# Optimization experiments

Hardware: AMD Instinct MI355X
Metric: run time of the kernel (lower is better)

Reference implementation:

```python
import jax, jax.numpy as jnp
import numpy as np

B, NEG = 2, 16            # queries, negatives per query
N, E, D = 10000, 80000, 128  # nodes, edges, feature dim (in_dim == out_dim)
NUM_REL = 237
L = 3                     # PNA layers
NODE_RATIO = 0.1
K = max(1, int(NODE_RATIO * N))  # static top-k: every repeated graph has exactly N nodes
EPS = 1e-5


def _score(hidden, rel, lin_W, lin_b, m1_W, m1_b, m2_W, m2_b):
    heur = jnp.concatenate([hidden, rel], axis=-1) @ lin_W + lin_b
    x = heur * hidden
    h = jax.nn.relu(x @ m1_W + m1_b)
    return jnp.squeeze(h @ m2_W + m2_b, -1)


def _pna_conv(hidden, src, dst, emask, deg, pre_W, pre_b, post_W, post_b, out_W, out_b):
    """PNA layer with mean/max/min/std aggregators and identity/amplification/attenuation
    scalers, restricted to edges where emask is True. deg is the (clamped >=1) degree used
    by the scalers."""
    BN = hidden.shape[0]
    # message: pre-linear on [x_i (target), x_j (source)] per edge  -> (Erep, D)
    m = jnp.concatenate([hidden[dst], hidden[src]], axis=-1) @ pre_W + pre_b
    w = emask.astype(hidden.dtype)[:, None]
    cnt = jax.ops.segment_sum(emask.astype(hidden.dtype), dst, num_segments=BN)
    denom = jnp.maximum(cnt, 1.0)[:, None]
    s1 = jax.ops.segment_sum(m * w, dst, num_segments=BN)
    s2 = jax.ops.segment_sum(m * m * w, dst, num_segments=BN)
    mean = s1 / denom
    var = jax.nn.relu(s2 / denom - mean * mean)
    std = jnp.sqrt(var + EPS)
    has = (cnt > 0)[:, None]
    mx = jnp.where(has, jax.ops.segment_max(jnp.where(emask[:, None], m, -jnp.inf), dst, num_segments=BN), 0.0)
    mn = jnp.where(has, jax.ops.segment_min(jnp.where(emask[:, None], m, jnp.inf), dst, num_segments=BN), 0.0)
    agg = jnp.concatenate([mean, mx, mn, std], axis=-1)           # (BN, 4D)
    logd = jnp.log(deg + 1.0)                                     # deg >= 1 -> logd > 0
    avg_log = jnp.mean(logd)
    agg = jnp.concatenate([agg, agg * (logd / avg_log)[:, None], agg * (avg_log / logd)[:, None]], axis=-1)  # (BN, 12D)
    return (agg @ post_W + post_b) @ out_W + out_b


def _forward(h_index, r_index, t_index, hidden_states, edge_index, rel_embedding,
             lin_W, lin_b, m1_W, m1_b, m2_W, m2_b, pre_W, pre_b, post_W, post_b, out_W, out_b):
    sc = (lin_W, lin_b, m1_W, m1_b, m2_W, m2_b)
    # negative_sample_to_tail
    is_t_neg = jnp.all(h_index == h_index[:, :1], axis=-1, keepdims=True)
    h_idx = jnp.where(is_t_neg, h_index, t_index)
    t_idx = jnp.where(is_t_neg, t_index, h_index)
    r_idx = jnp.where(is_t_neg, r_index, r_index + NUM_REL)
    # repeat_graph
    offsets = jnp.arange(B, dtype=h_idx.dtype) * N               # (B,)
    src = jnp.tile(edge_index[0], B) + jnp.repeat(offsets, E)    # (B*E,)
    dst = jnp.tile(edge_index[1], B) + jnp.repeat(offsets, E)
    BN = B * N
    rel_embeds = rel_embedding[r_idx[:, 0]].astype(hidden_states.dtype)  # (B, D)
    flat_h = h_idx[:, 0] + offsets
    flat_t = t_idx[:, 0] + offsets
    # literal `repeat_interleave(N, dim=0)[:B]` quirk -> row arange(B)//N of gathered embs
    sel = jnp.arange(B) // N
    h_vals = hidden_states[h_idx[:, 0]][sel]                     # (B, D)
    t_vals = hidden_states[t_idx[:, 0]][sel]
    # init_input_embeds: boundary condition + initial score at head nodes
    boundary = jnp.zeros((BN, D), hidden_states.dtype).at[flat_t].set(t_vals).at[flat_h].set(h_vals)
    score = jnp.zeros(BN, jnp.float32).at[flat_h].set(_score(h_vals, rel_embeds, *sc))
    hidden = boundary
    rel_per_node = jnp.repeat(rel_embeds, N, axis=0)             # (BN, D), rel_embeds[batch_rep]
    rows = jnp.arange(B)[:, None]
    for l in range(L):
        # select_edges_pyg with degree_ratio=1.0: all out-edges of per-graph top-k nodes
        _, idx = jax.lax.top_k(score.reshape(B, N), K)           # (B, K)
        node_sel = jnp.zeros((B, N), bool).at[rows, idx].set(True).reshape(-1)
        emask = node_sel[src]                                    # (B*E,) selected-edge mask
        out_deg = jax.ops.segment_sum(emask.astype(jnp.float32), src, num_segments=BN)
        deg_sub = jnp.maximum(out_deg.astype(hidden.dtype), 1.0)
        new_hidden = _pna_conv(hidden, src, dst, emask, deg_sub,
                               pre_W[l], pre_b[l], post_W[l], post_b[l], out_W[l], out_b[l])
        # residual only for nodes with selected outgoing edges
        hidden = jnp.where((out_deg > 0)[:, None], hidden + new_hidden, hidden)
        score = _score(hidden, rel_per_node, *sc)
    # read out scores at (repeated) tail indices -> (B, NEG)
    return score[t_idx + offsets[:, None]]


def setup_inputs() -> dict:
    key = jax.random.key(0)
    ks = jax.random.split(key, 14)
    s = 0.05
    hi = jax.random.randint(ks[0], (B, 1), 0, N)
    h_index = jnp.tile(hi, (1, NEG))                 # constant per row (assert in forward)
    r0 = jax.random.randint(ks[1], (B, 1), 0, NUM_REL)
    r_index = jnp.tile(r0, (1, NEG))                 # constant per row (assert in forward)
    t_index = jax.random.randint(ks[2], (B, NEG), 0, N)
    hidden_states = jax.random.normal(ks[3], (N, D), jnp.float32)
    edge_index = jax.random.randint(ks[4], (2, E), 0, N)
    return {
        "h_index": h_index, "r_index": r_index, "t_index": t_index,
        "hidden_states": hidden_states, "edge_index": edge_index,
        "rel_embedding": jax.random.normal(ks[5], (2 * NUM_REL, D), jnp.float32) * s,
        "lin_W": jax.random.normal(ks[6], (2 * D, D), jnp.float32) * s, "lin_b": jnp.zeros(D, jnp.float32),
        "m1_W": jax.random.normal(ks[7], (D, D), jnp.float32) * s, "m1_b": jnp.zeros(D, jnp.float32),
        "m2_W": jax.random.normal(ks[8], (D, 1), jnp.float32) * s, "m2_b": jnp.zeros(1, jnp.float32),
        "pre_W": jax.random.normal(ks[9], (L, 2 * D, D), jnp.float32) * s, "pre_b": jnp.zeros((L, D), jnp.float32),
        "post_W": jax.random.normal(ks[10], (L, 12 * D, D), jnp.float32) * s, "post_b": jnp.zeros((L, D), jnp.float32),
        "out_W": jax.random.normal(ks[11], (L, D, D), jnp.float32) * s, "out_b": jnp.zeros((L, D), jnp.float32),
    }


def reference(h_index, r_index, t_index, hidden_states, edge_index, rel_embedding,
              lin_W, lin_b, m1_W, m1_b, m2_W, m2_b, pre_W, pre_b, post_W, post_b, out_W, out_b):
    return _forward(h_index, r_index, t_index, hidden_states, edge_index, rel_embedding,
                    lin_W, lin_b, m1_W, m1_b, m2_W, m2_b, pre_W, pre_b, post_W, post_b, out_W, out_b)
```

## Files before the change

### kernel.cpp

```cpp
#include <hip/hip_runtime.h>
#include <math.h>

#define Bq 2
#define NEG 16
#define Nn 10000
#define Ee 80000
#define Dd 128
#define NUM_REL 237
#define Ll 3
#define K_SEL 1000
#define BN (Bq*Nn)
#define EPSV 1e-5f
#define MAXACT 2048
#define MAXTOUCH 8192
#define SELCAP 3328
#define LN2F 0.69314718056f

constexpr size_t HID_OFF   = 0;
constexpr size_t SCORE_OFF = HID_OFF   + (size_t)BN*Dd*4;
constexpr size_t CVEC_OFF  = SCORE_OFF + (size_t)BN*4;
constexpr size_t HDR_OFF   = CVEC_OFF  + (size_t)Bq*Dd*4;
constexpr size_t THR_OFF   = HDR_OFF   + 64*4;
constexpr size_t SEL_OFF   = THR_OFF   + Bq*8;
constexpr size_t DEG_OFF   = SEL_OFF   + (size_t)BN*4;
constexpr size_t SLOT_OFF  = DEG_OFF   + (size_t)BN*4;
constexpr size_t CNT_OFF   = SLOT_OFF  + (size_t)BN*4;
constexpr size_t SDEG_OFF  = CNT_OFF   + (size_t)MAXACT*4;
constexpr size_t S1_OFF    = SDEG_OFF  + (size_t)MAXACT*4;
constexpr size_t S2_OFF    = S1_OFF    + (size_t)MAXACT*Dd*4;
constexpr size_t MXB_OFF   = S2_OFF    + (size_t)MAXACT*Dd*4;
constexpr size_t MNB_OFF   = MXB_OFF   + (size_t)MAXACT*Dd*4;
constexpr size_t TPART_OFF = MNB_OFF   + (size_t)MAXACT*Dd*4;
constexpr size_t ALIST_OFF = TPART_OFF + (size_t)4*MAXACT*Dd*4;
constexpr size_t FLAG_OFF  = ALIST_OFF + (size_t)MAXACT*4;
constexpr size_t TLIST_OFF = FLAG_OFF  + (size_t)BN*4;
constexpr size_t EDGE_OFF  = TLIST_OFF + (size_t)MAXTOUCH*4;
constexpr size_t CTR_OFF   = EDGE_OFF  + (size_t)Bq*Ee*2*4;

__device__ __forceinline__ unsigned encf(float f){
  unsigned u = __float_as_uint(f);
  return (u & 0x80000000u) ? ~u : (u | 0x80000000u);
}
__device__ __forceinline__ float decf(unsigned e){
  unsigned u = (e & 0x80000000u) ? (e & 0x7FFFFFFFu) : ~e;
  return __uint_as_float(u);
}
__device__ __forceinline__ unsigned long long make_key(float f, int i){
  unsigned d = ~encf(f);
  return ((unsigned long long)d << 32) | (unsigned)i;
}

__global__ void k_zero(float* hidden, unsigned* flag){
  int i = blockIdx.x*blockDim.x + threadIdx.x;
  if (i < BN*Dd/4) ((float4*)hidden)[i] = make_float4(0.f,0.f,0.f,0.f);
  if (i < BN) flag[i] = 0u;
}

__global__ __launch_bounds__(256) void k_prep(
    const int* h_index, const int* r_index, const int* t_index,
    const float* hidden_states, const float* rel_embedding,
    const float* lin_W, const float* lin_b, const float* m1_W, const float* m1_b,
    const float* m2_W, const float* m2_b,
    int* hdr, float* cvec, float* hidden, float* score,
    unsigned* flag, int* tlist, unsigned* ctr){
  __shared__ int sh_fh[Bq], sh_ft[Bq], sh_r0[Bq], sh_hsrc, sh_tsrc;
  __shared__ float s_relv[Bq][Dd], s_cvec[Bq][Dd], s_hv[Dd], s_x[Bq][Dd], s_p[Bq][Dd];
  __shared__ float s_s0[Dd];
  __shared__ float sc0_sh;
  int tid = threadIdx.x;
  if (tid == 0){
    int n = 0;
    for (int b=0;b<Bq;b++){
      bool eq = true;
      for (int j=1;j<NEG;j++) eq = eq && (h_index[b*NEG+j]==h_index[b*NEG]);
      int h0 = eq ? h_index[b*NEG] : t_index[b*NEG];
      int t0 = eq ? t_index[b*NEG] : h_index[b*NEG];
      int r0 = eq ? r_index[b*NEG] : r_index[b*NEG] + NUM_REL;
      sh_fh[b] = h0 + b*Nn; sh_ft[b] = t0 + b*Nn; sh_r0[b] = r0;
      hdr[0+b] = sh_fh[b]; hdr[2+b] = sh_ft[b];
      for (int j=0;j<NEG;j++){
        int tj = eq ? t_index[b*NEG+j] : h_index[b*NEG+j];
        hdr[4 + b*NEG + j] = tj + b*Nn;
      }
      if (b==0){ sh_hsrc = h0; sh_tsrc = t0; }
      if (!flag[sh_ft[b]]){ flag[sh_ft[b]] = 1u; tlist[n++] = sh_ft[b]; }
      if (!flag[sh_fh[b]]){ flag[sh_fh[b]] = 1u; tlist[n++] = sh_fh[b]; }
    }
    ctr[3] = (unsigned)n;
  }
  __syncthreads();
  int b = tid >> 7, d = tid & 127;
  s_relv[b][d] = rel_embedding[(size_t)sh_r0[b]*Dd + d];
  if (b == 0){
    s_hv[d] = hidden_states[(size_t)sh_hsrc*Dd + d];
    s_s0[d] = fmaxf(m1_b[d], 0.f) * m2_W[d];
  }
  __syncthreads();
  if (tid == 0){
    float s = m2_b[0];
    for (int k=0;k<Dd;k++) s += s_s0[k];
    sc0_sh = s;
    ctr[4] = __float_as_uint(s);
  }
  float acc = lin_b[d];
  #pragma unroll 8
  for (int k=0;k<Dd;k++) acc += s_relv[b][k]*lin_W[(Dd+k)*Dd + d];
  s_cvec[b][d] = acc; cvec[b*Dd+d] = acc;
  hidden[(size_t)sh_ft[b]*Dd + d] = hidden_states[(size_t)sh_tsrc*Dd + d];
  hidden[(size_t)sh_fh[b]*Dd + d] = hidden_states[(size_t)sh_hsrc*Dd + d];
  __syncthreads();
  float sc0 = sc0_sh;
  for (int i = tid; i < BN; i += 256) score[i] = sc0;
  float hv = s_hv[d];
  float heur = s_cvec[b][d];
  #pragma unroll 8
  for (int k=0;k<Dd;k++) heur += s_hv[k]*lin_W[k*Dd + d];
  s_x[b][d] = heur * hv;
  __syncthreads();
  float a2 = m1_b[d];
  #pragma unroll 8
  for (int k=0;k<Dd;k++) a2 += s_x[b][k]*m1_W[k*Dd + d];
  s_p[b][d] = fmaxf(a2, 0.f) * m2_W[d];
  __syncthreads();
  if (tid < Bq){
    float s = m2_b[0];
    for (int k=0;k<Dd;k++) s += s_p[tid][k];
    score[sh_fh[tid]] = s;
  }
}

__global__ __launch_bounds__(256) void k_select(
    const float* score, const int* tlist, const unsigned* ctr,
    unsigned long long* thr){
  int b = blockIdx.x;
  int nt = (int)ctr[3];
  unsigned d0 = ~encf(__uint_as_float(ctr[4]));
  __shared__ unsigned sd[SELCAP];
  __shared__ unsigned short sidx[SELCAP];
  __shared__ unsigned hist[256], histT[256];
  __shared__ int ntb_sh;
  __shared__ unsigned long long pref_sh;
  __shared__ unsigned kk_sh;
  int tid = threadIdx.x;
  if (tid==0){ ntb_sh = 0; pref_sh = 0ull; kk_sh = K_SEL; }
  __syncthreads();
  int vlo = b*Nn, vhi = vlo + Nn;
  for (int i = tid; i < nt; i += 256){
    int v = tlist[i];
    if (v >= vlo && v < vhi){
      int pos = atomicAdd(&ntb_sh, 1);
      if (pos < SELCAP){
        sd[pos] = ~encf(score[v]);
        sidx[pos] = (unsigned short)(v - vlo);
      }
    }
  }
  __syncthreads();
  int ntb = min(ntb_sh, SELCAP);
  unsigned nvirt = (unsigned)(Nn - ntb);
  for (int pass = 7; pass >= 0; --pass){
    hist[tid] = 0u; histT[tid] = 0u;
    __syncthreads();
    unsigned long long pref = pref_sh;
    int sh_hi = 8*(pass+1);
    for (int j = tid; j < ntb; j += 256){
      unsigned long long key = ((unsigned long long)sd[j] << 32) | (unsigned long long)sidx[j];
      bool ok = (pass==7) || ((key >> sh_hi) == (pref >> sh_hi));
      if (ok) atomicAdd(&hist[(unsigned)(key >> (8*pass)) & 255u], 1u);
      if (pass < 4){
        unsigned idx = sidx[j];
        bool oki = (pass == 3) || ((idx >> sh_hi) == (((unsigned)pref) >> sh_hi));
        if (oki) atomicAdd(&histT[(idx >> (8*pass)) & 255u], 1u);
      }
    }
    __syncthreads();
    if (pass >= 4){
      if (tid == 0){
        unsigned long long keyv_hi = ((unsigned long long)d0 << 32);
        bool ok = (pass==7) || ((keyv_hi >> sh_hi) == (pref >> sh_hi));
        if (ok) atomicAdd(&hist[(d0 >> (8*(pass-4))) & 255u], nvirt);
      }
    } else {
      if ((unsigned)(pref >> 32) == d0){
        unsigned long long hf = 0ull;
        if (pass < 3) hf = (unsigned long long)((((unsigned)pref) >> sh_hi)) << sh_hi;
        unsigned long long lo = hf + ((unsigned long long)tid << (8*pass));
        unsigned long long hi = lo + (1ull << (8*pass));
        unsigned long long nn = (unsigned long long)Nn;
        unsigned long long l2 = lo < nn ? lo : nn;
        unsigned long long h2 = hi < nn ? hi : nn;
        if (h2 > l2){
          unsigned c = (unsigned)(h2 - l2) - histT[tid];
          if (c > 0u) atomicAdd(&hist[tid], c);
        }
      }
    }
    __syncthreads();
    if (tid < 256){
      unsigned kk = kk_sh;
      unsigned cum = 0;
      for (int i=0;i<tid;i++) cum += hist[i];
      unsigned h = hist[tid];
      if (h > 0u && cum < kk && kk <= cum + h){
        pref_sh |= ((unsigned long long)tid) << (8*pass);
        kk_sh = kk - cum;
      }
    }
    __syncthreads();
  }
  if (tid==0) thr[b] = pref_sh;
}

__global__ void k_mask(const float* score, const unsigned long long* thr, unsigned* sel,
                       unsigned* out_deg, float* s1, float* s2,
                       unsigned* mxb, unsigned* mnb, unsigned* cnt, unsigned* ctr){
  int i = blockIdx.x*blockDim.x + threadIdx.x;
  if (i < BN){
    int b = i / Nn; int v = i - b*Nn;
    sel[i] = (make_key(score[i], v) <= thr[b]) ? 1u : 0u;
    out_deg[i] = 0u;
  }
  if (i < MAXACT*Dd){ s1[i]=0.f; s2[i]=0.f; mxb[i]=0u; mnb[i]=0xFFFFFFFFu; }
  if (i < MAXACT) cnt[i]=0u;
  if (i < 3) ctr[i]=0u;
}

__global__ void k_degree(const int* ei, const unsigned* sel, unsigned* out_deg){
  int e = blockIdx.x*blockDim.x + threadIdx.x;
  if (e >= Ee) return;
  int s0 = ei[e];
  #pragma unroll
  for (int b=0;b<Bq;b++){
    int v = s0 + b*Nn;
    if (sel[v]) atomicAdd(&out_deg[v], 1u);
  }
}

__global__ void k_active(const unsigned* out_deg, int* node_slot, int* alist,
                         float* slot_deg, unsigned* ctr, unsigned* flag, int* tlist){
  int v = blockIdx.x*blockDim.x + threadIdx.x;
  if (v >= BN) return;
  unsigned dg = out_deg[v];
  if (dg > 0u){
    int slot = (int)atomicAdd(&ctr[0], 1u);
    alist[slot] = v; node_slot[v] = slot; slot_deg[slot] = (float)dg;
    atomicAdd((float*)&ctr[2], logf((float)dg + 1.0f));
    if (atomicExch(&flag[v], 1u) == 0u){
      int p = (int)atomicAdd(&ctr[3], 1u);
      tlist[p] = v;
    }
  }
}

__global__ void k_edges(const int* ei, const unsigned* sel, const unsigned* out_deg,
                        const int* node_slot, int* edges, unsigned* cnt, unsigned* ctr){
  int e = blockIdx.x*blockDim.x + threadIdx.x;
  if (e >= Ee) return;
  int s0 = ei[e], d0 = ei[Ee + e];
  #pragma unroll
  for (int b=0;b<Bq;b++){
    int s = s0 + b*Nn, dv = d0 + b*Nn;
    if (sel[s] && out_deg[dv] > 0u){
      int slot = node_slot[dv];
      int j = (int)atomicAdd(&ctr[1], 1u);
      edges[2*j] = s; edges[2*j+1] = slot;
      atomicAdd(&cnt[slot], 1u);
    }
  }
}

__global__ __launch_bounds__(128) void k_messages(
    const float* hidden, const int* edges, const int* alist,
    const float* preW, const float* preb,
    float* s1, float* s2, unsigned* mxb, unsigned* mnb, const unsigned* ctr){
  int ne = (int)ctr[1];
  int tid = threadIdx.x;
  __shared__ float sd[4][Dd], ss[4][Dd];
  __shared__ int dsl[4];
  float pb = preb[tid];
  for (int j0 = blockIdx.x*4; j0 < ne; j0 += gridDim.x*4){
    int nv = ne - j0; if (nv > 4) nv = 4;
    if (tid < 4){
      int j = j0 + ((tid < nv) ? tid : 0);
      dsl[tid] = edges[2*j+1];
    }
    #pragma unroll
    for (int e=0;e<4;e++){
      int j = j0 + ((e < nv) ? e : 0);
      int s = edges[2*j];
      int dv = alist[edges[2*j+1]];
      sd[e][tid] = hidden[(size_t)dv*Dd + tid];
      ss[e][tid] = hidden[(size_t)s*Dd + tid];
    }
    __syncthreads();
    float a[4] = {pb, pb, pb, pb};
    #pragma unroll 4
    for (int k=0;k<Dd;k++){
      float w0 = preW[k*Dd + tid];
      float w1 = preW[(Dd+k)*Dd + tid];
      #pragma unroll
      for (int e=0;e<4;e++) a[e] += sd[e][k]*w0 + ss[e][k]*w1;
    }
    for (int e=0;e<nv;e++){
      int dslot = dsl[e];
      atomicAdd(&s1[dslot*Dd + tid], a[e]);
      atomicAdd(&s2[dslot*Dd + tid], a[e]*a[e]);
      atomicMax(&mxb[dslot*Dd + tid], encf(a[e]));
      atomicMin(&mnb[dslot*Dd + tid], encf(a[e]));
    }
    __syncthreads();
  }
}

__global__ __launch_bounds__(512) void k_post(
    const unsigned* cnt, const float* s1, const float* s2,
    const unsigned* mxb, const unsigned* mnb, const float* slot_deg,
    const float* postW, float* tpart, const unsigned* ctr){
  int na = (int)ctr[0];
  int bid = blockIdx.x;
  int tile = bid & 63, ch = bid >> 6;
  if (tile*32 >= na) return;
  float logsum = __uint_as_float(ctr[2]);
  float avg = (logsum + (float)(BN - na)*LN2F) / (float)BN;
  __shared__ float lb[32*136];
  __shared__ float wbuf[3*16*128];
  __shared__ float sden[32];
  __shared__ unsigned shas[32];
  int tid = threadIdx.x;
  if (tid < 32){
    unsigned c = cnt[tile*32 + tid];
    sden[tid] = fmaxf((float)c, 1.0f);
    shas[tid] = c;
  }
  __syncthreads();
  for (int idx = tid; idx < 32*Dd; idx += 512){
    int sl = idx >> 7, kk = idx & 127;
    int gi = (tile*32 + sl)*Dd + kk;
    float den = sden[sl];
    float val;
    if (ch == 0)      val = s1[gi]/den;
    else if (ch == 1) val = shas[sl] ? decf(mxb[gi]) : 0.f;
    else if (ch == 2) val = shas[sl] ? decf(mnb[gi]) : 0.f;
    else {
      float mv = s1[gi]/den;
      float var = s2[gi]/den - mv*mv;
      val = sqrtf(fmaxf(var, 0.f) + EPSV);
    }
    lb[sl*136 + kk] = val;
  }
  int cg = tid & 31, rg = tid >> 5;
  int c0 = cg*4;
  float a0[2][4], a1[2][4], a2[2][4];
  #pragma unroll
  for (int i=0;i<2;i++)
    #pragma unroll
    for (int j=0;j<4;j++){ a0[i][j]=0.f; a1[i][j]=0.f; a2[i][j]=0.f; }
  for (int chunk = 0; chunk < 8; ++chunk){
    #pragma unroll
    for (int i = 0; i < 3; ++i){
      int f = tid + i*512;
      int q = f >> 9, r = f & 511;
      int kk = r >> 5, c4 = r & 31;
      int grow = q*512 + ch*128 + chunk*16 + kk;
      ((float4*)wbuf)[f] = *(const float4*)(postW + (size_t)grow*Dd + c4*4);
    }
    __syncthreads();
    #pragma unroll
    for (int k4 = 0; k4 < 4; ++k4){
      float4 av0 = *(const float4*)&lb[(rg*2+0)*136 + chunk*16 + k4*4];
      float4 av1 = *(const float4*)&lb[(rg*2+1)*136 + chunk*16 + k4*4];
      #pragma unroll
      for (int j = 0; j < 4; ++j){
        int kk = k4*4 + j;
        float4 w0 = *(const float4*)&wbuf[kk*128 + c0];
        float4 w1 = *(const float4*)&wbuf[(16+kk)*128 + c0];
        float4 w2 = *(const float4*)&wbuf[(32+kk)*128 + c0];
        float av[2] = { (&av0.x)[j], (&av1.x)[j] };
        #pragma unroll
        for (int i=0;i<2;i++){
          float a = av[i];
          a0[i][0] += a*w0.x; a0[i][1] += a*w0.y; a0[i][2] += a*w0.z; a0[i][3] += a*w0.w;
          a1[i][0] += a*w1.x; a1[i][1] += a*w1.y; a1[i][2] += a*w1.z; a1[i][3] += a*w1.w;
          a2[i][0] += a*w2.x; a2[i][1] += a*w2.y; a2[i][2] += a*w2.z; a2[i][3] += a*w2.w;
        }
      }
    }
    __syncthreads();
  }
  #pragma unroll
  for (int i=0;i<2;i++){
    int slot = tile*32 + rg*2 + i;
    if (slot < na){
      float dg = slot_deg[slot];
      float logd = logf(dg + 1.f);
      float al = logd/avg, be = avg/logd;
      float4 r;
      r.x = a0[i][0] + al*a1[i][0] + be*a2[i][0];
      r.y = a0[i][1] + al*a1[i][1] + be*a2[i][1];
      r.z = a0[i][2] + al*a1[i][2] + be*a2[i][2];
      r.w = a0[i][3] + al*a1[i][3] + be*a2[i][3];
      *(float4*)(tpart + (size_t)ch*MAXACT*Dd + (size_t)slot*Dd + c0) = r;
    }
  }
}

__global__ __launch_bounds__(256) void k_out_resid(
    const float* tpart, const int* alist, const float* outW, const float* outb,
    const float* postb, float* hidden, const unsigned* ctr){
  int na = (int)ctr[0];
  int tile = blockIdx.x;
  if (tile*32 >= na) return;
  __shared__ float tr[32*136];
  __shared__ float wbuf[16*128];
  int tid = threadIdx.x;
  for (int idx = tid; idx < 32*Dd; idx += 256){
    int sl = idx >> 7, kk = idx & 127;
    size_t o = (size_t)(tile*32 + sl)*Dd + kk;
    tr[sl*136 + kk] = tpart[o] + tpart[(size_t)MAXACT*Dd + o]
                    + tpart[(size_t)2*MAXACT*Dd + o] + tpart[(size_t)3*MAXACT*Dd + o]
                    + postb[kk];
  }
  int cg = tid & 31, rg = tid >> 5;
  int c0 = cg*4;
  float4 ob = *(const float4*)(outb + c0);
  float acc[4][4];
  #pragma unroll
  for (int r=0;r<4;r++){ acc[r][0]=ob.x; acc[r][1]=ob.y; acc[r][2]=ob.z; acc[r][3]=ob.w; }
  for (int chunk = 0; chunk < 8; ++chunk){
    #pragma unroll
    for (int i = 0; i < 2; ++i){
      int f = tid + i*256;
      int kk = f >> 5, c4 = f & 31;
      ((float4*)wbuf)[f] = *(const float4*)(outW + (size_t)(chunk*16 + kk)*Dd + c4*4);
    }
    __syncthreads();
    #pragma unroll
    for (int k4 = 0; k4 < 4; ++k4){
      float4 av[4];
      #pragma unroll
      for (int r=0;r<4;r++)
        av[r] = *(const float4*)&tr[(rg*4+r)*136 + chunk*16 + k4*4];
      #pragma unroll
      for (int j = 0; j < 4; ++j){
        float4 w = *(const float4*)&wbuf[(k4*4+j)*128 + c0];
        #pragma unroll
        for (int r=0;r<4;r++){
          float a = (&av[r].x)[j];
          acc[r][0] += a*w.x; acc[r][1] += a*w.y; acc[r][2] += a*w.z; acc[r][3] += a*w.w;
        }
      }
    }
    __syncthreads();
  }
  #pragma unroll
  for (int r=0;r<4;r++){
    int slot = tile*32 + rg*4 + r;
    if (slot < na){
      int v = alist[slot];
      float* hp = hidden + (size_t)v*Dd + c0;
      float4 h4 = *(float4*)hp;
      h4.x += acc[r][0]; h4.y += acc[r][1]; h4.z += acc[r][2]; h4.w += acc[r][3];
      *(float4*)hp = h4;
    }
  }
}

__global__ __launch_bounds__(256) void k_score(
    const float* hidden, const float* cvec, const float* linW,
    const float* m1W, const float* m1b, const float* m2W, const float* m2b,
    const int* tlist, const unsigned* ctr, float* score,
    const int* ovr, int ovr_n){
  int nt = (ovr_n > 0) ? ovr_n : (int)ctr[3];
  const int* list = (ovr_n > 0) ? ovr : tlist;
  int nb = blockIdx.x * 32;
  if (nb >= nt) return;
  __shared__ float sh[32*Dd];
  __shared__ float sx[32*Dd];
  __shared__ float sc[2*Dd];
  __shared__ int   sv[32];
  __shared__ float red[32*33];
  int tid = threadIdx.x;
  if (tid < 32){
    int idx = nb + tid;
    sv[tid] = (idx < nt) ? list[idx] : list[nb];
  }
  sc[tid] = cvec[tid];
  __syncthreads();
  for (int q = tid; q < 32*32; q += 256){
    int row = q >> 5, f4 = q & 31;
    ((float4*)sh)[row*32 + f4] = ((const float4*)(hidden + (size_t)sv[row]*Dd))[f4];
  }
  __syncthreads();
  int cg = tid & 31, rg = tid >> 5;
  int c0 = cg*4;
  float acc[4][4];
  #pragma unroll
  for (int i=0;i<4;i++){ acc[i][0]=0.f; acc[i][1]=0.f; acc[i][2]=0.f; acc[i][3]=0.f; }
  for (int k4=0;k4<32;k4++){
    float4 av[4];
    #pragma unroll
    for (int i=0;i<4;i++) av[i] = ((float4*)sh)[(rg*4+i)*32 + k4];
    #pragma unroll
    for (int j=0;j<4;j++){
      float4 w = *(const float4*)(linW + (size_t)(k4*4+j)*Dd + c0);
      #pragma unroll
      for (int i=0;i<4;i++){
        float a = (&av[i].x)[j];
        acc[i][0] += a*w.x; acc[i][1] += a*w.y; acc[i][2] += a*w.z; acc[i][3] += a*w.w;
      }
    }
  }
  #pragma unroll
  for (int i=0;i<4;i++){
    int row = rg*4 + i;
    int bb = (sv[row] >= Nn) ? 1 : 0;
    float4 cv = *(float4*)&sc[bb*Dd + c0];
    float4 hv = ((float4*)sh)[row*32 + cg];
    float4 x;
    x.x = (acc[i][0] + cv.x)*hv.x;
    x.y = (acc[i][1] + cv.y)*hv.y;
    x.z = (acc[i][2] + cv.z)*hv.z;
    x.w = (acc[i][3] + cv.w)*hv.w;
    ((float4*)sx)[row*32 + cg] = x;
  }
  __syncthreads();
  #pragma unroll
  for (int i=0;i<4;i++){ acc[i][0]=0.f; acc[i][1]=0.f; acc[i][2]=0.f; acc[i][3]=0.f; }
  for (int k4=0;k4<32;k4++){
    float4 av[4];
    #pragma unroll
    for (int i=0;i<4;i++) av[i] = ((float4*)sx)[(rg*4+i)*32 + k4];
    #pragma unroll
    for (int j=0;j<4;j++){
      float4 w = *(const float4*)(m1W + (size_t)(k4*4+j)*Dd + c0);
      #pragma unroll
      for (int i=0;i<4;i++){
        float a = (&av[i].x)[j];
        acc[i][0] += a*w.x; acc[i][1] += a*w.y; acc[i][2] += a*w.z; acc[i][3] += a*w.w;
      }
    }
  }
  float4 mb = *(const float4*)(m1b + c0);
  float4 mw = *(const float4*)(m2W + c0);
  #pragma unroll
  for (int i=0;i<4;i++){
    float p0 = fmaxf(acc[i][0]+mb.x, 0.f)*mw.x;
    float p1 = fmaxf(acc[i][1]+mb.y, 0.f)*mw.y;
    float p2 = fmaxf(acc[i][2]+mb.z, 0.f)*mw.z;
    float p3 = fmaxf(acc[i][3]+mb.w, 0.f)*mw.w;
    red[(rg*4+i)*33 + cg] = p0+p1+p2+p3;
  }
  __syncthreads();
  if (tid < 32){
    float s = m2b[0];
    for (int g=0; g<32; g++) s += red[tid*33 + g];
    if (nb + tid < nt) score[sv[tid]] = s;
  }
}

__global__ void k_gather(const float* score, const int* hdr, float* out){
  int i = threadIdx.x;
  if (i < Bq*NEG) out[i] = score[hdr[4+i]];
}

extern "C" void kernel_launch(void* const* d_in, const int* in_sizes, int n_in,
                              void* d_out, int out_size, void* d_ws, size_t ws_size,
                              hipStream_t stream){
  const int*   h_index       = (const int*)d_in[0];
  const int*   r_index       = (const int*)d_in[1];
  const int*   t_index       = (const int*)d_in[2];
  const float* hidden_states = (const float*)d_in[3];
  const int*   edge_index    = (const int*)d_in[4];
  const float* rel_embedding = (const float*)d_in[5];
  const float* lin_W  = (const float*)d_in[6];
  const float* lin_b  = (const float*)d_in[7];
  const float* m1_W   = (const float*)d_in[8];
  const float* m1_b   = (const float*)d_in[9];
  const float* m2_W   = (const float*)d_in[10];
  const float* m2_b   = (const float*)d_in[11];
  const float* pre_W  = (const float*)d_in[12];
  const float* pre_b  = (const float*)d_in[13];
  const float* post_W = (const float*)d_in[14];
  const float* post_b = (const float*)d_in[15];
  const float* out_W  = (const float*)d_in[16];
  const float* out_b  = (const float*)d_in[17];

  char* ws = (char*)d_ws;
  float*    hidden   = (float*)(ws + HID_OFF);
  float*    score    = (float*)(ws + SCORE_OFF);
  float*    cvec     = (float*)(ws + CVEC_OFF);
  int*      hdr      = (int*)(ws + HDR_OFF);
  unsigned long long* thr = (unsigned long long*)(ws + THR_OFF);
  unsigned* sel      = (unsigned*)(ws + SEL_OFF);
  unsigned* out_deg  = (unsigned*)(ws + DEG_OFF);
  int*      node_slot= (int*)(ws + SLOT_OFF);
  unsigned* cnt      = (unsigned*)(ws + CNT_OFF);
  float*    slot_deg = (float*)(ws + SDEG_OFF);
  float*    s1       = (float*)(ws + S1_OFF);
  float*    s2       = (float*)(ws + S2_OFF);
  unsigned* mxb      = (unsigned*)(ws + MXB_OFF);
  unsigned* mnb      = (unsigned*)(ws + MNB_OFF);
  float*    tpart    = (float*)(ws + TPART_OFF);
  int*      alist    = (int*)(ws + ALIST_OFF);
  unsigned* flag     = (unsigned*)(ws + FLAG_OFF);
  int*      tlist    = (int*)(ws + TLIST_OFF);
  int*      edges    = (int*)(ws + EDGE_OFF);
  unsigned* ctr      = (unsigned*)(ws + CTR_OFF);

  k_zero<<<(BN*Dd/4 + 255)/256, 256, 0, stream>>>(hidden, flag);
  k_prep<<<1, 256, 0, stream>>>(h_index, r_index, t_index, hidden_states, rel_embedding,
                                lin_W, lin_b, m1_W, m1_b, m2_W, m2_b,
                                hdr, cvec, hidden, score, flag, tlist, ctr);
  for (int l = 0; l < Ll; ++l){
    const float* preWl  = pre_W  + (size_t)l*2*Dd*Dd;
    const float* prebl  = pre_b  + (size_t)l*Dd;
    const float* postWl = post_W + (size_t)l*12*Dd*Dd;
    const float* postbl = post_b + (size_t)l*Dd;
    const float* outWl  = out_W  + (size_t)l*Dd*Dd;
    const float* outbl  = out_b  + (size_t)l*Dd;

    k_select<<<Bq, 256, 0, stream>>>(score, tlist, ctr, thr);
    k_mask<<<(MAXACT*Dd + 255)/256, 256, 0, stream>>>(score, thr, sel, out_deg,
                                                      s1, s2, mxb, mnb, cnt, ctr);
    k_degree<<<(Ee + 255)/256, 256, 0, stream>>>(edge_index, sel, out_deg);
    k_active<<<(BN + 255)/256, 256, 0, stream>>>(out_deg, node_slot, alist, slot_deg,
                                                 ctr, flag, tlist);
    k_edges<<<(Ee + 255)/256, 256, 0, stream>>>(edge_index, sel, out_deg, node_slot,
                                                edges, cnt, ctr);
    k_messages<<<512, 128, 0, stream>>>(hidden, edges, alist, preWl, prebl,
                                        s1, s2, mxb, mnb, ctr);
    k_post<<<256, 512, 0, stream>>>(cnt, s1, s2, mxb, mnb, slot_deg, postWl, tpart, ctr);
    k_out_resid<<<MAXACT/32, 256, 0, stream>>>(tpart, alist, outWl, outbl, postbl,
                                               hidden, ctr);
    if (l < Ll-1){
      k_score<<<MAXTOUCH/32, 256, 0, stream>>>(hidden, cvec, lin_W, m1_W, m1_b, m2_W, m2_b,
                                               tlist, ctr, score, tlist, 0);
    } else {
      k_score<<<1, 256, 0, stream>>>(hidden, cvec, lin_W, m1_W, m1_b, m2_W, m2_b,
                                     tlist, ctr, score, hdr + 4, Bq*NEG);
    }
  }
  k_gather<<<1, 64, 0, stream>>>(score, hdr, (float*)d_out);
}
```

Before: 481.7 us.

## Fuse all per-layer kernels into one persistent cooperative kernel with grid syncs

Replaces the sequence of roughly ten kernel launches per layer with a single persistent cooperative kernel that uses grid-wide syncs between phases. Launch gaps and the separate zeroing and gather kernels go away, and the selection phase overlaps with the accumulator clearing on the other blocks. Phases are reworked as grid-stride loops over a fixed grid of 256 or 512 blocks, and the per-node select mask is replaced by recomputing keys from the threshold. The cost is many grid.sync barriers, a fixed grid size for every phase, and shared-memory unions that may limit occupancy.

New measurement: 1.262 ms. +162.0%, slower.

```diff
diff --git a/kernel.cpp b/kernel.cpp
--- a/kernel.cpp
+++ b/kernel.cpp
@@ -1,5 +1,8 @@
 #include <hip/hip_runtime.h>
+#include <hip/hip_cooperative_groups.h>
 #include <math.h>
+
+namespace cg = cooperative_groups;
 
 #define Bq 2
 #define NEG 16
@@ -50,517 +53,565 @@
   return ((unsigned long long)d << 32) | (unsigned)i;
 }
 
-__global__ void k_zero(float* hidden, unsigned* flag){
-  int i = blockIdx.x*blockDim.x + threadIdx.x;
-  if (i < BN*Dd/4) ((float4*)hidden)[i] = make_float4(0.f,0.f,0.f,0.f);
-  if (i < BN) flag[i] = 0u;
-}
-
-__global__ __launch_bounds__(256) void k_prep(
-    const int* h_index, const int* r_index, const int* t_index,
-    const float* hidden_states, const float* rel_embedding,
-    const float* lin_W, const float* lin_b, const float* m1_W, const float* m1_b,
-    const float* m2_W, const float* m2_b,
-    int* hdr, float* cvec, float* hidden, float* score,
-    unsigned* flag, int* tlist, unsigned* ctr){
-  __shared__ int sh_fh[Bq], sh_ft[Bq], sh_r0[Bq], sh_hsrc, sh_tsrc;
-  __shared__ float s_relv[Bq][Dd], s_cvec[Bq][Dd], s_hv[Dd], s_x[Bq][Dd], s_p[Bq][Dd];
-  __shared__ float s_s0[Dd];
-  __shared__ float sc0_sh;
-  int tid = threadIdx.x;
+union __align__(16) SM {
+  struct {
+    int hbuf[Bq*NEG], tbuf[Bq*NEG], rbuf[Bq*NEG];
+    int fh[Bq], ft[Bq], r0[Bq], eqf[Bq], hsrc, tsrc;
+    float s0red[Dd]; float sc0;
+    float relv[Bq][Dd], cv[Bq][Dd], hv[Dd], x[Bq][Dd], p[Bq][Dd];
+  } prep;
+  struct {
+    unsigned sd[SELCAP];
+    unsigned short sidx[SELCAP];
+    unsigned hist[256], histT[256];
+    int ntb; unsigned kk; unsigned long long pref;
+  } sel;
+  struct { float sd[8][Dd], ss[8][Dd]; } msg;
+  struct { float lb[32*136], wbuf[3*16*128], sden[32]; unsigned shas[32]; } post;
+  struct { float tr[32*136], wbuf[16*128]; } outr;
+  struct { float sh[32*Dd], sx[32*Dd], sc[2*Dd], red[32*33]; int sv[32]; } score;
+};
+
+__global__ __launch_bounds__(256, 2) void k_main(
+    const int* __restrict__ h_index, const int* __restrict__ r_index, const int* __restrict__ t_index,
+    const float* __restrict__ hidden_states, const int* __restrict__ edge_index,
+    const float* __restrict__ rel_embedding,
+    const float* __restrict__ lin_W, const float* __restrict__ lin_b,
+    const float* __restrict__ m1_W, const float* __restrict__ m1_b,
+    const float* __restrict__ m2_W, const float* __restrict__ m2_b,
+    const float* __restrict__ pre_W, const float* __restrict__ pre_b,
+    const float* __restrict__ post_W, const float* __restrict__ post_b,
+    const float* __restrict__ out_W, const float* __restrict__ out_b,
+    char* __restrict__ ws, float* __restrict__ out)
+{
+  float*    hidden   = (float*)(ws + HID_OFF);
+  float*    score    = (float*)(ws + SCORE_OFF);
+  float*    cvec     = (float*)(ws + CVEC_OFF);
+  int*      hdr      = (int*)(ws + HDR_OFF);
+  unsigned long long* thr = (unsigned long long*)(ws + THR_OFF);
+  unsigned* out_deg  = (unsigned*)(ws + DEG_OFF);
+  int*      node_slot= (int*)(ws + SLOT_OFF);
+  unsigned* cnt      = (unsigned*)(ws + CNT_OFF);
+  float*    slot_deg = (float*)(ws + SDEG_OFF);
+  float*    s1       = (float*)(ws + S1_OFF);
+  float*    s2       = (float*)(ws + S2_OFF);
+  unsigned* mxb      = (unsigned*)(ws + MXB_OFF);
+  unsigned* mnb      = (unsigned*)(ws + MNB_OFF);
+  float*    tpart    = (float*)(ws + TPART_OFF);
+  int*      alist    = (int*)(ws + ALIST_OFF);
+  unsigned* flag     = (unsigned*)(ws + FLAG_OFF);
+  int*      tlist    = (int*)(ws + TLIST_OFF);
+  int*      edges    = (int*)(ws + EDGE_OFF);
+  unsigned* ctr      = (unsigned*)(ws + CTR_OFF);
+
+  cg::grid_group gg = cg::this_grid();
+  __shared__ SM sm;
+  const int tid  = threadIdx.x;
+  const int bid  = blockIdx.x;
+  const int gsz  = gridDim.x * 256;
+  const int gtid = bid * 256 + tid;
+
+  if (tid < Bq*NEG){
+    sm.prep.hbuf[tid] = h_index[tid];
+    sm.prep.tbuf[tid] = t_index[tid];
+    sm.prep.rbuf[tid] = r_index[tid];
+  }
+  if (tid < Dd) sm.prep.s0red[tid] = fmaxf(m1_b[tid], 0.f) * m2_W[tid];
+  __syncthreads();
   if (tid == 0){
-    int n = 0;
-    for (int b=0;b<Bq;b++){
+    for (int b = 0; b < Bq; b++){
       bool eq = true;
-      for (int j=1;j<NEG;j++) eq = eq && (h_index[b*NEG+j]==h_index[b*NEG]);
-      int h0 = eq ? h_index[b*NEG] : t_index[b*NEG];
-      int t0 = eq ? t_index[b*NEG] : h_index[b*NEG];
-      int r0 = eq ? r_index[b*NEG] : r_index[b*NEG] + NUM_REL;
-      sh_fh[b] = h0 + b*Nn; sh_ft[b] = t0 + b*Nn; sh_r0[b] = r0;
-      hdr[0+b] = sh_fh[b]; hdr[2+b] = sh_ft[b];
-      for (int j=0;j<NEG;j++){
-        int tj = eq ? t_index[b*NEG+j] : h_index[b*NEG+j];
-        hdr[4 + b*NEG + j] = tj + b*Nn;
-      }
-      if (b==0){ sh_hsrc = h0; sh_tsrc = t0; }
-      if (!flag[sh_ft[b]]){ flag[sh_ft[b]] = 1u; tlist[n++] = sh_ft[b]; }
-      if (!flag[sh_fh[b]]){ flag[sh_fh[b]] = 1u; tlist[n++] = sh_fh[b]; }
-    }
-    ctr[3] = (unsigned)n;
+      for (int j = 1; j < NEG; j++) eq = eq && (sm.prep.hbuf[b*NEG+j] == sm.prep.hbuf[b*NEG]);
+      int h0 = eq ? sm.prep.hbuf[b*NEG] : sm.prep.tbuf[b*NEG];
+      int t0 = eq ? sm.prep.tbuf[b*NEG] : sm.prep.hbuf[b*NEG];
+      int r0 = eq ? sm.prep.rbuf[b*NEG] : sm.prep.rbuf[b*NEG] + NUM_REL;
+      sm.prep.fh[b] = h0 + b*Nn; sm.prep.ft[b] = t0 + b*Nn;
+      sm.prep.r0[b] = r0; sm.prep.eqf[b] = eq ? 1 : 0;
+      if (b == 0){ sm.prep.hsrc = h0; sm.prep.tsrc = t0; }
+    }
+    float s = m2_b[0];
+    for (int k = 0; k < Dd; k++) s += sm.prep.s0red[k];
+    sm.prep.sc0 = s;
+    if (bid == 0){
+      ctr[4] = __float_as_uint(s);
+      hdr[0] = sm.prep.fh[0]; hdr[1] = sm.prep.fh[1];
+      hdr[2] = sm.prep.ft[0]; hdr[3] = sm.prep.ft[1];
+      for (int b = 0; b < Bq; b++)
+        for (int j = 0; j < NEG; j++){
+          int tj = sm.prep.eqf[b] ? sm.prep.tbuf[b*NEG+j] : sm.prep.hbuf[b*NEG+j];
+          hdr[4 + b*NEG + j] = tj + b*Nn;
+        }
+      int cand[4] = { sm.prep.ft[0], sm.prep.fh[0], sm.prep.ft[1], sm.prep.fh[1] };
+      int n = 0;
+      for (int c = 0; c < 4; c++){
+        bool dup = false;
+        for (int m = 0; m < n; m++) dup = dup || (tlist[m] == cand[c]);
+        if (!dup) tlist[n++] = cand[c];
+        flag[cand[c]] = 1u;
+      }
+      ctr[3] = (unsigned)n;
+    }
   }
   __syncthreads();
-  int b = tid >> 7, d = tid & 127;
-  s_relv[b][d] = rel_embedding[(size_t)sh_r0[b]*Dd + d];
-  if (b == 0){
-    s_hv[d] = hidden_states[(size_t)sh_hsrc*Dd + d];
-    s_s0[d] = fmaxf(m1_b[d], 0.f) * m2_W[d];
+  {
+    const int fh0 = sm.prep.fh[0], fh1 = sm.prep.fh[1];
+    const int ft0 = sm.prep.ft[0], ft1 = sm.prep.ft[1];
+    const float sc0 = sm.prep.sc0;
+    if (bid == 0){
+      int b = tid >> 7, d = tid & 127;
+      sm.prep.relv[b][d] = rel_embedding[(size_t)sm.prep.r0[b]*Dd + d];
+      if (b == 0) sm.prep.hv[d] = hidden_states[(size_t)sm.prep.hsrc*Dd + d];
+      __syncthreads();
+      float acc = lin_b[d];
+      #pragma unroll 8
+      for (int k = 0; k < Dd; k++) acc += sm.prep.relv[b][k]*lin_W[(Dd+k)*Dd + d];
+      sm.prep.cv[b][d] = acc; cvec[b*Dd + d] = acc;
+      hidden[(size_t)sm.prep.ft[b]*Dd + d] = hidden_states[(size_t)sm.prep.tsrc*Dd + d];
+      hidden[(size_t)sm.prep.fh[b]*Dd + d] = hidden_states[(size_t)sm.prep.hsrc*Dd + d];
+      __syncthreads();
+      float hv = sm.prep.hv[d];
+      float heur = sm.prep.cv[b][d];
+      #pragma unroll 8
+      for (int k = 0; k < Dd; k++) heur += sm.prep.hv[k]*lin_W[k*Dd + d];
+      sm.prep.x[b][d] = heur * hv;
+      __syncthreads();
+      float a2 = m1_b[d];
+      #pragma unroll 8
+      for (int k = 0; k < Dd; k++) a2 += sm.prep.x[b][k]*m1_W[k*Dd + d];
+      sm.prep.p[b][d] = fmaxf(a2, 0.f) * m2_W[d];
+      __syncthreads();
+      if (tid < Bq){
+        float s = m2_b[0];
+        for (int k = 0; k < Dd; k++) s += sm.prep.p[tid][k];
+        score[sm.prep.fh[tid]] = s;
+      }
+    } else {
+      int zb = bid - 1, znb = gridDim.x - 1;
+      int zt = zb*256 + tid, zs = znb*256;
+      float4 z4 = make_float4(0.f, 0.f, 0.f, 0.f);
+      for (int i = zt; i < BN*32; i += zs){
+        int row = i >> 5;
+        if (row != ft0 && row != ft1 && row != fh0 && row != fh1)
+          ((float4*)hidden)[i] = z4;
+      }
+      for (int v = zt; v < BN; v += zs){
+        if (v != ft0 && v != ft1 && v != fh0 && v != fh1) flag[v] = 0u;
+        if (v != fh0 && v != fh1) score[v] = sc0;
+      }
+    }
   }
-  __syncthreads();
-  if (tid == 0){
-    float s = m2_b[0];
-    for (int k=0;k<Dd;k++) s += s_s0[k];
-    sc0_sh = s;
-    ctr[4] = __float_as_uint(s);
+  gg.sync();
+
+  for (int l = 0; l < Ll; ++l){
+    const float* preWl  = pre_W  + (size_t)l*2*Dd*Dd;
+    const float* prebl  = pre_b  + (size_t)l*Dd;
+    const float* postWl = post_W + (size_t)l*12*Dd*Dd;
+    const float* postbl = post_b + (size_t)l*Dd;
+    const float* outWl  = out_W  + (size_t)l*Dd*Dd;
+    const float* outbl  = out_b  + (size_t)l*Dd;
+
+    if (bid < Bq){
+      int b = bid;
+      int nt = (int)ctr[3];
+      unsigned d0 = ~encf(__uint_as_float(ctr[4]));
+      if (tid == 0){ sm.sel.ntb = 0; sm.sel.pref = 0ull; sm.sel.kk = K_SEL; }
+      __syncthreads();
+      int vlo = b*Nn, vhi = vlo + Nn;
+      for (int i = tid; i < nt; i += 256){
+        int v = tlist[i];
+        if (v >= vlo && v < vhi){
+          int pos = atomicAdd(&sm.sel.ntb, 1);
+          if (pos < SELCAP){
+            sm.sel.sd[pos] = ~encf(score[v]);
+            sm.sel.sidx[pos] = (unsigned short)(v - vlo);
+          }
+        }
+      }
+      __syncthreads();
+      int ntb = min(sm.sel.ntb, SELCAP);
+      unsigned nvirt = (unsigned)(Nn - ntb);
+      for (int pass = 7; pass >= 0; --pass){
+        sm.sel.hist[tid] = 0u; sm.sel.histT[tid] = 0u;
+        __syncthreads();
+        unsigned long long pref = sm.sel.pref;
+        int sh_hi = 8*(pass+1);
+        for (int j = tid; j < ntb; j += 256){
+          unsigned long long key = ((unsigned long long)sm.sel.sd[j] << 32) | (unsigned long long)sm.sel.sidx[j];
+          bool ok = (pass==7) || ((key >> sh_hi) == (pref >> sh_hi));
+          if (ok) atomicAdd(&sm.sel.hist[(unsigned)(key >> (8*pass)) & 255u], 1u);
+          if (pass < 4){
+            unsigned idx = sm.sel.sidx[j];
+            bool oki = (pass == 3) || ((idx >> sh_hi) == (((unsigned)pref) >> sh_hi));
+            if (oki) atomicAdd(&sm.sel.histT[(idx >> (8*pass)) & 255u], 1u);
+          }
+        }
+        __syncthreads();
+        if (pass >= 4){
+          if (tid == 0){
+            unsigned long long keyv_hi = ((unsigned long long)d0 << 32);
+            bool ok = (pass==7) || ((keyv_hi >> sh_hi) == (sm.sel.pref >> sh_hi));
+            if (ok) atomicAdd(&sm.sel.hist[(d0 >> (8*(pass-4))) & 255u], nvirt);
+          }
+        } else {
+          if ((unsigned)(pref >> 32) == d0){
+            unsigned long long hf = 0ull;
+            if (pass < 3) hf = (unsigned long long)((((unsigned)pref) >> sh_hi)) << sh_hi;
+            unsigned long long lo = hf + ((unsigned long long)tid << (8*pass));
+            unsigned long long hi = lo + (1ull << (8*pass));
+            unsigned long long nn = (unsigned long long)Nn;
+            unsigned long long l2 = lo < nn ? lo : nn;
+            unsigned long long h2 = hi < nn ? hi : nn;
+            if (h2 > l2){
+              unsigned c = (unsigned)(h2 - l2) - sm.sel.histT[tid];
+              if (c > 0u) atomicAdd(&sm.sel.hist[tid], c);
+            }
+          }
+        }
+        __syncthreads();
+        {
+          unsigned kk = sm.sel.kk;
+          unsigned cum = 0;
+          for (int i = 0; i < tid; i++) cum += sm.sel.hist[i];
+          unsigned h = sm.sel.hist[tid];
+          if (h > 0u && cum < kk && kk <= cum + h){
+            sm.sel.pref |= ((unsigned long long)tid) << (8*pass);
+            sm.sel.kk = kk - cum;
+          }
+        }
+        __syncthreads();
+      }
+      if (tid == 0) thr[b] = sm.sel.pref;
+    } else {
+      int zb = bid - Bq, znb = gridDim.x - Bq;
+      int zt = zb*256 + tid, zs = znb*256;
+      for (int i = zt; i < MAXACT*Dd; i += zs){
+        s1[i] = 0.f; s2[i] = 0.f; mxb[i] = 0u; mnb[i] = 0xFFFFFFFFu;
+      }
+      for (int i = zt; i < BN; i += zs) out_deg[i] = 0u;
+      for (int i = zt; i < MAXACT; i += zs) cnt[i] = 0u;
+      if (zt < 3) ctr[zt] = 0u;
+    }
+    gg.sync();
+
+    {
+      unsigned long long th0 = thr[0], th1 = thr[1];
+      for (int e = gtid; e < Ee; e += gsz){
+        int s0 = edge_index[e];
+        if (make_key(score[s0], s0) <= th0) atomicAdd(&out_deg[s0], 1u);
+        int v1 = s0 + Nn;
+        if (make_key(score[v1], s0) <= th1) atomicAdd(&out_deg[v1], 1u);
+      }
+    }
+    gg.sync();
+
+    for (int v = gtid; v < BN; v += gsz){
+      unsigned dg = out_deg[v];
+      if (dg > 0u){
+        int slot = (int)atomicAdd(&ctr[0], 1u);
+        alist[slot] = v; node_slot[v] = slot; slot_deg[slot] = (float)dg;
+        atomicAdd((float*)&ctr[2], logf((float)dg + 1.0f));
+        if (atomicExch(&flag[v], 1u) == 0u){
+          int p = (int)atomicAdd(&ctr[3], 1u);
+          tlist[p] = v;
+        }
+      }
+    }
+    gg.sync();
+
+    {
+      unsigned long long th0 = thr[0], th1 = thr[1];
+      for (int e = gtid; e < Ee; e += gsz){
+        int s0 = edge_index[e], d0e = edge_index[Ee + e];
+        #pragma unroll
+        for (int b = 0; b < Bq; b++){
+          int s = s0 + b*Nn, dv = d0e + b*Nn;
+          unsigned long long th = b ? th1 : th0;
+          if (make_key(score[s], s0) <= th && out_deg[dv] > 0u){
+            int slot = node_slot[dv];
+            int j = (int)atomicAdd(&ctr[1], 1u);
+            edges[2*j] = s; edges[2*j+1] = slot;
+            atomicAdd(&cnt[slot], 1u);
+          }
+        }
+      }
+    }
+    gg.sync();
+
+    {
+      int ne = (int)ctr[1];
+      int half = tid >> 7, d = tid & 127;
+      float pb = prebl[d];
+      for (int j0 = bid*8; j0 < ne; j0 += gridDim.x*8){
+        int base = j0 + half*4;
+        int nv = ne - base; if (nv > 4) nv = 4; if (nv < 0) nv = 0;
+        int dsl[4];
+        #pragma unroll
+        for (int e = 0; e < 4; e++){
+          int j = (e < nv) ? base + e : j0;
+          int s = edges[2*j]; int slot = edges[2*j+1];
+          dsl[e] = slot;
+          int dv = alist[slot];
+          sm.msg.sd[half*4+e][d] = hidden[(size_t)dv*Dd + d];
+          sm.msg.ss[half*4+e][d] = hidden[(size_t)s*Dd + d];
+        }
+        __syncthreads();
+        float a[4] = {pb, pb, pb, pb};
+        #pragma unroll 4
+        for (int k = 0; k < Dd; k++){
+          float w0 = preWl[k*Dd + d];
+          float w1 = preWl[(Dd+k)*Dd + d];
+          #pragma unroll
+          for (int e = 0; e < 4; e++)
+            a[e] += sm.msg.sd[half*4+e][k]*w0 + sm.msg.ss[half*4+e][k]*w1;
+        }
+        for (int e = 0; e < nv; e++){
+          int dslot = dsl[e];
+          atomicAdd(&s1[dslot*Dd + d], a[e]);
+          atomicAdd(&s2[dslot*Dd + d], a[e]*a[e]);
+          atomicMax(&mxb[dslot*Dd + d], encf(a[e]));
+          atomicMin(&mnb[dslot*Dd + d], encf(a[e]));
+        }
+        __syncthreads();
+      }
+    }
+    gg.sync();
+
+    {
+      int na = (int)ctr[0];
+      int ntile = (na + 31) >> 5;
+      float logsum = __uint_as_float(ctr[2]);
+      float avg = (logsum + (float)(BN - na)*LN2F) / (float)BN;
+      for (int w = bid; w < ntile*4; w += gridDim.x){
+        int tile = w % ntile, ch = w / ntile;
+        if (tid < 32){
+          unsigned c = cnt[tile*32 + tid];
+          sm.post.sden[tid] = fmaxf((float)c, 1.0f);
+          sm.post.shas[tid] = c;
+        }
+        __syncthreads();
+        for (int idx = tid; idx < 32*Dd; idx += 256){
+          int sl = idx >> 7, kk = idx & 127;
+          int gi = (tile*32 + sl)*Dd + kk;
+          float den = sm.post.sden[sl];
+          float val;
+          if (ch == 0)      val = s1[gi]/den;
+          else if (ch == 1) val = sm.post.shas[sl] ? decf(mxb[gi]) : 0.f;
+          else if (ch == 2) val = sm.post.shas[sl] ? decf(mnb[gi]) : 0.f;
+          else {
+            float mv = s1[gi]/den;
+            float var = s2[gi]/den - mv*mv;
+            val = sqrtf(fmaxf(var, 0.f) + EPSV);
+          }
+          sm.post.lb[sl*136 + kk] = val;
+        }
+        int cgp = tid & 31, rg = tid >> 5;
+        int c0 = cgp*4;
+        float a0[4][4], a1[4][4], a2[4][4];
+        #pragma unroll
+        for (int i = 0; i < 4; i++)
+          #pragma unroll
+          for (int j = 0; j < 4; j++){ a0[i][j]=0.f; a1[i][j]=0.f; a2[i][j]=0.f; }
+        for (int chunk = 0; chunk < 8; ++chunk){
+          #pragma unroll
+          for (int i2 = 0; i2 < 6; ++i2){
+            int f = tid + i2*256;
+            int q = f >> 9, r = f & 511;
+            int kk = r >> 5, c4 = r & 31;
+            int grow = q*512 + ch*128 + chunk*16 + kk;
+            ((float4*)sm.post.wbuf)[f] = *(const float4*)(postWl + (size_t)grow*Dd + c4*4);
+          }
+          __syncthreads();
+          #pragma unroll
+          for (int k4 = 0; k4 < 4; ++k4){
+            float4 av[4];
+            #pragma unroll
+            for (int i = 0; i < 4; i++)
+              av[i] = *(const float4*)&sm.post.lb[(rg*4+i)*136 + chunk*16 + k4*4];
+            #pragma unroll
+            for (int j = 0; j < 4; ++j){
+              int kk = k4*4 + j;
+              float4 w0 = *(const float4*)&sm.post.wbuf[kk*128 + c0];
+              float4 w1 = *(const float4*)&sm.post.wbuf[(16+kk)*128 + c0];
+              float4 w2 = *(const float4*)&sm.post.wbuf[(32+kk)*128 + c0];
+              #pragma unroll
+              for (int i = 0; i < 4; i++){
+                float a = (&av[i].x)[j];
+                a0[i][0] += a*w0.x; a0[i][1] += a*w0.y; a0[i][2] += a*w0.z; a0[i][3] += a*w0.w;
+                a1[i][0] += a*w1.x; a1[i][1] += a*w1.y; a1[i][2] += a*w1.z; a1[i][3] += a*w1.w;
+                a2[i][0] += a*w2.x; a2[i][1] += a*w2.y; a2[i][2] += a*w2.z; a2[i][3] += a*w2.w;
+              }
+            }
+          }
+          __syncthreads();
+        }
+        #pragma unroll
+        for (int i = 0; i < 4; i++){
+          int slot = tile*32 + rg*4 + i;
+          if (slot < na){
+            float dg = slot_deg[slot];
+            float logd = logf(dg + 1.f);
+            float al = logd/avg, be = avg/logd;
+            float4 r;
+            r.x = a0[i][0] + al*a1[i][0] + be*a2[i][0];
+            r.y = a0[i][1] + al*a1[i][1] + be*a2[i][1];
+            r.z = a0[i][2] + al*a1[i][2] + be*a2[i][2];
+            r.w = a0[i][3] + al*a1[i][3] + be*a2[i][3];
+            *(float4*)(tpart + (size_t)ch*MAXACT*Dd + (size_t)slot*Dd + c0) = r;
+          }
+        }
+        __syncthreads();
+      }
+    }
+    gg.sync();
+
+    {
+      int na = (int)ctr[0];
+      int ntile = (na + 31) >> 5;
+      for (int tile = bid; tile < ntile; tile += gridDim.x){
+        for (int idx = tid; idx < 32*Dd; idx += 256){
+          int sl = idx >> 7, kk = idx & 127;
+          size_t o = (size_t)(tile*32 + sl)*Dd + kk;
+          sm.outr.tr[sl*136 + kk] = tpart[o] + tpart[(size_t)MAXACT*Dd + o]
+                                  + tpart[(size_t)2*MAXACT*Dd + o] + tpart[(size_t)3*MAXACT*Dd + o]
+                                  + postbl[kk];
+        }
+        int cgp = tid & 31, rg = tid >> 5;
+        int c0 = cgp*4;
+        float4 ob = *(const float4*)(outbl + c0);
+        float acc[4][4];
+        #pragma unroll
+        for (int r = 0; r < 4; r++){ acc[r][0]=ob.x; acc[r][1]=ob.y; acc[r][2]=ob.z; acc[r][3]=ob.w; }
+        for (int chunk = 0; chunk < 8; ++chunk){
+          #pragma unroll
+          for (int i2 = 0; i2 < 2; ++i2){
+            int f = tid + i2*256;
+            int kk = f >> 5, c4 = f & 31;
+            ((float4*)sm.outr.wbuf)[f] = *(const float4*)(outWl + (size_t)(chunk*16 + kk)*Dd + c4*4);
+          }
+          __syncthreads();
+          #pragma unroll
+          for (int k4 = 0; k4 < 4; ++k4){
+            float4 av[4];
+            #pragma unroll
+            for (int r = 0; r < 4; r++)
+              av[r] = *(const float4*)&sm.outr.tr[(rg*4+r)*136 + chunk*16 + k4*4];
+            #pragma unroll
+            for (int j = 0; j < 4; ++j){
+              float4 w = *(const float4*)&sm.outr.wbuf[(k4*4+j)*128 + c0];
+              #pragma unroll
+              for (int r = 0; r < 4; r++){
+                float a = (&av[r].x)[j];
+                acc[r][0] += a*w.x; acc[r][1] += a*w.y; acc[r][2] += a*w.z; acc[r][3] += a*w.w;
+              }
+            }
+          }
+          __syncthreads();
+        }
+        #pragma unroll
+        for (int r = 0; r < 4; r++){
+          int slot = tile*32 + rg*4 + r;
+          if (slot < na){
+            int v = alist[slot];
+            float* hp = hidden + (size_t)v*Dd + c0;
+            float4 h4 = *(float4*)hp;
+            h4.x += acc[r][0]; h4.y += acc[r][1]; h4.z += acc[r][2]; h4.w += acc[r][3];
+            *(float4*)hp = h4;
+          }
+        }
+        __syncthreads();
+      }
+    }
+    gg.sync();
+
+    {
+      const int* list; int nt;
+      if (l < Ll-1){ list = tlist; nt = (int)ctr[3]; }
+      else         { list = hdr + 4; nt = Bq*NEG; }
+      for (int t = bid; t*32 < nt; t += gridDim.x){
+        int nb = t*32;
+        if (tid < 32){
+          int idx = nb + tid;
+          sm.score.sv[tid] = (idx < nt) ? list[idx] : list[nb];
+        }
+        sm.score.sc[tid] = cvec[tid];
+        __syncthreads();
+        for (int q = tid; q < 32*32; q += 256){
+          int row = q >> 5, f4 = q & 31;
+          ((float4*)sm.score.sh)[row*32 + f4] = ((const float4*)(hidden + (size_t)sm.score.sv[row]*Dd))[f4];
+        }
+        __syncthreads();
+        int cgp = tid & 31, rg = tid >> 5;
+        int c0 = cgp*4;
+        float acc[4][4];
+        #pragma unroll
+        for (int i = 0; i < 4; i++){ acc[i][0]=0.f; acc[i][1]=0.f; acc[i][2]=0.f; acc[i][3]=0.f; }
+        for (int k4 = 0; k4 < 32; k4++){
+          float4 av[4];
+          #pragma unroll
+          for (int i = 0; i < 4; i++) av[i] = ((float4*)sm.score.sh)[(rg*4+i)*32 + k4];
+          #pragma unroll
+          for (int j = 0; j < 4; j++){
+            float4 w = *(const float4*)(lin_W + (size_t)(k4*4+j)*Dd + c0);
+            #pragma unroll
+            for (int i = 0; i < 4; i++){
+              float a = (&av[i].x)[j];
+              acc[i][0] += a*w.x; acc[i][1] += a*w.y; acc[i][2] += a*w.z; acc[i][3] += a*w.w;
+            }
+          }
+        }
+        #pragma unroll
+        for (int i = 0; i < 4; i++){
+          int row = rg*4 + i;
+          int bb = (sm.score.sv[row] >= Nn) ? 1 : 0;
+          float4 cv = *(float4*)&sm.score.sc[bb*Dd + c0];
+          float4 hv = ((float4*)sm.score.sh)[row*32 + cgp];
+          float4 x;
+          x.x = (acc[i][0] + cv.x)*hv.x;
+          x.y = (acc[i][1] + cv.y)*hv.y;
+          x.z = (acc[i][2] + cv.z)*hv.z;
+          x.w = (acc[i][3] + cv.w)*hv.w;
+          ((float4*)sm.score.sx)[row*32 + cgp] = x;
+        }
+        __syncthreads();
+        #pragma unroll
+        for (int i = 0; i < 4; i++){ acc[i][0]=0.f; acc[i][1]=0.f; acc[i][2]=0.f; acc[i][3]=0.f; }
+        for (int k4 = 0; k4 < 32; k4++){
+          float4 av[4];
+          #pragma unroll
+          for (int i = 0; i < 4; i++) av[i] = ((float4*)sm.score.sx)[(rg*4+i)*32 + k4];
+          #pragma unroll
+          for (int j = 0; j < 4; j++){
+            float4 w = *(const float4*)(m1_W + (size_t)(k4*4+j)*Dd + c0);
+            #pragma unroll
+            for (int i = 0; i < 4; i++){
+              float a = (&av[i].x)[j];
+              acc[i][0] += a*w.x; acc[i][1] += a*w.y; acc[i][2] += a*w.z; acc[i][3] += a*w.w;
+            }
+          }
+        }
+        float4 mb = *(const float4*)(m1_b + c0);
+        float4 mw = *(const float4*)(m2_W + c0);
+        #pragma unroll
+        for (int i = 0; i < 4; i++){
+          float p0 = fmaxf(acc[i][0]+mb.x, 0.f)*mw.x;
+          float p1 = fmaxf(acc[i][1]+mb.y, 0.f)*mw.y;
+          float p2 = fmaxf(acc[i][2]+mb.z, 0.f)*mw.z;
+          float p3 = fmaxf(acc[i][3]+mb.w, 0.f)*mw.w;
+          sm.score.red[(rg*4+i)*33 + cgp] = p0+p1+p2+p3;
+        }
+        __syncthreads();
+        if (tid < 32){
+          float s = m2_b[0];
+          for (int g = 0; g < 32; g++) s += sm.score.red[tid*33 + g];
+          if (nb + tid < nt) score[sm.score.sv[tid]] = s;
+        }
+        __syncthreads();
+      }
+    }
+    gg.sync();
   }
-  float acc = lin_b[d];
-  #pragma unroll 8
-  for (int k=0;k<Dd;k++) acc += s_relv[b][k]*lin_W[(Dd+k)*Dd + d];
-  s_cvec[b][d] = acc; cvec[b*Dd+d] = acc;
-  hidden[(size_t)sh_ft[b]*Dd + d] = hidden_states[(size_t)sh_tsrc*Dd + d];
-  hidden[(size_t)sh_fh[b]*Dd + d] = hidden_states[(size_t)sh_hsrc*Dd + d];
-  __syncthreads();
-  float sc0 = sc0_sh;
-  for (int i = tid; i < BN; i += 256) score[i] = sc0;
-  float hv = s_hv[d];
-  float heur = s_cvec[b][d];
-  #pragma unroll 8
-  for (int k=0;k<Dd;k++) heur += s_hv[k]*lin_W[k*Dd + d];
-  s_x[b][d] = heur * hv;
-  __syncthreads();
-  float a2 = m1_b[d];
-  #pragma unroll 8
-  for (int k=0;k<Dd;k++) a2 += s_x[b][k]*m1_W[k*Dd + d];
-  s_p[b][d] = fmaxf(a2, 0.f) * m2_W[d];
-  __syncthreads();
-  if (tid < Bq){
-    float s = m2_b[0];
-    for (int k=0;k<Dd;k++) s += s_p[tid][k];
-    score[sh_fh[tid]] = s;
-  }
-}
-
-__global__ __launch_bounds__(256) void k_select(
-    const float* score, const int* tlist, const unsigned* ctr,
-    unsigned long long* thr){
-  int b = blockIdx.x;
-  int nt = (int)ctr[3];
-  unsigned d0 = ~encf(__uint_as_float(ctr[4]));
-  __shared__ unsigned sd[SELCAP];
-  __shared__ unsigned short sidx[SELCAP];
-  __shared__ unsigned hist[256], histT[256];
-  __shared__ int ntb_sh;
-  __shared__ unsigned long long pref_sh;
-  __shared__ unsigned kk_sh;
-  int tid = threadIdx.x;
-  if (tid==0){ ntb_sh = 0; pref_sh = 0ull; kk_sh = K_SEL; }
-  __syncthreads();
-  int vlo = b*Nn, vhi = vlo + Nn;
-  for (int i = tid; i < nt; i += 256){
-    int v = tlist[i];
-    if (v >= vlo && v < vhi){
-      int pos = atomicAdd(&ntb_sh, 1);
-      if (pos < SELCAP){
-        sd[pos] = ~encf(score[v]);
-        sidx[pos] = (unsigned short)(v - vlo);
-      }
-    }
-  }
-  __syncthreads();
-  int ntb = min(ntb_sh, SELCAP);
-  unsigned nvirt = (unsigned)(Nn - ntb);
-  for (int pass = 7; pass >= 0; --pass){
-    hist[tid] = 0u; histT[tid] = 0u;
-    __syncthreads();
-    unsigned long long pref = pref_sh;
-    int sh_hi = 8*(pass+1);
-    for (int j = tid; j < ntb; j += 256){
-      unsigned long long key = ((unsigned long long)sd[j] << 32) | (unsigned long long)sidx[j];
-      bool ok = (pass==7) || ((key >> sh_hi) == (pref >> sh_hi));
-      if (ok) atomicAdd(&hist[(unsigned)(key >> (8*pass)) & 255u], 1u);
-      if (pass < 4){
-        unsigned idx = sidx[j];
-        bool oki = (pass == 3) || ((idx >> sh_hi) == (((unsigned)pref) >> sh_hi));
-        if (oki) atomicAdd(&histT[(idx >> (8*pass)) & 255u], 1u);
-      }
-    }
-    __syncthreads();
-    if (pass >= 4){
-      if (tid == 0){
-        unsigned long long keyv_hi = ((unsigned long long)d0 << 32);
-        bool ok = (pass==7) || ((keyv_hi >> sh_hi) == (pref >> sh_hi));
-        if (ok) atomicAdd(&hist[(d0 >> (8*(pass-4))) & 255u], nvirt);
-      }
-    } else {
-      if ((unsigned)(pref >> 32) == d0){
-        unsigned long long hf = 0ull;
-        if (pass < 3) hf = (unsigned long long)((((unsigned)pref) >> sh_hi)) << sh_hi;
-        unsigned long long lo = hf + ((unsigned long long)tid << (8*pass));
-        unsigned long long hi = lo + (1ull << (8*pass));
-        unsigned long long nn = (unsigned long long)Nn;
-        unsigned long long l2 = lo < nn ? lo : nn;
-        unsigned long long h2 = hi < nn ? hi : nn;
-        if (h2 > l2){
-          unsigned c = (unsigned)(h2 - l2) - histT[tid];
-          if (c > 0u) atomicAdd(&hist[tid], c);
-        }
-      }
-    }
-    __syncthreads();
-    if (tid < 256){
-      unsigned kk = kk_sh;
-      unsigned cum = 0;
-      for (int i=0;i<tid;i++) cum += hist[i];
-      unsigned h = hist[tid];
-      if (h > 0u && cum < kk && kk <= cum + h){
-        pref_sh |= ((unsigned long long)tid) << (8*pass);
-        kk_sh = kk - cum;
-      }
-    }
-    __syncthreads();
-  }
-  if (tid==0) thr[b] = pref_sh;
-}
-
-__global__ void k_mask(const float* score, const unsigned long long* thr, unsigned* sel,
-                       unsigned* out_deg, float* s1, float* s2,
-                       unsigned* mxb, unsigned* mnb, unsigned* cnt, unsigned* ctr){
-  int i = blockIdx.x*blockDim.x + threadIdx.x;
-  if (i < BN){
-    int b = i / Nn; int v = i - b*Nn;
-    sel[i] = (make_key(score[i], v) <= thr[b]) ? 1u : 0u;
-    out_deg[i] = 0u;
-  }
-  if (i < MAXACT*Dd){ s1[i]=0.f; s2[i]=0.f; mxb[i]=0u; mnb[i]=0xFFFFFFFFu; }
-  if (i < MAXACT) cnt[i]=0u;
-  if (i < 3) ctr[i]=0u;
-}
-
-__global__ void k_degree(const int* ei, const unsigned* sel, unsigned* out_deg){
-  int e = blockIdx.x*blockDim.x + threadIdx.x;
-  if (e >= Ee) return;
-  int s0 = ei[e];
-  #pragma unroll
-  for (int b=0;b<Bq;b++){
-    int v = s0 + b*Nn;
-    if (sel[v]) atomicAdd(&out_deg[v], 1u);
-  }
-}
-
-__global__ void k_active(const unsigned* out_deg, int* node_slot, int* alist,
-                         float* slot_deg, unsigned* ctr, unsigned* flag, int* tlist){
-  int v = blockIdx.x*blockDim.x + threadIdx.x;
-  if (v >= BN) return;
-  unsigned dg = out_deg[v];
-  if (dg > 0u){
-    int slot = (int)atomicAdd(&ctr[0], 1u);
-    alist[slot] = v; node_slot[v] = slot; slot_deg[slot] = (float)dg;
-    atomicAdd((float*)&ctr[2], logf((float)dg + 1.0f));
-    if (atomicExch(&flag[v], 1u) == 0u){
-      int p = (int)atomicAdd(&ctr[3], 1u);
-      tlist[p] = v;
-    }
-  }
-}
-
-__global__ void k_edges(const int* ei, const unsigned* sel, const unsigned* out_deg,
-                        const int* node_slot, int* edges, unsigned* cnt, unsigned* ctr){
-  int e = blockIdx.x*blockDim.x + threadIdx.x;
-  if (e >= Ee) return;
-  int s0 = ei[e], d0 = ei[Ee + e];
-  #pragma unroll
-  for (int b=0;b<Bq;b++){
-    int s = s0 + b*Nn, dv = d0 + b*Nn;
-    if (sel[s] && out_deg[dv] > 0u){
-      int slot = node_slot[dv];
-      int j = (int)atomicAdd(&ctr[1], 1u);
-      edges[2*j] = s; edges[2*j+1] = slot;
-      atomicAdd(&cnt[slot], 1u);
-    }
-  }
-}
-
-__global__ __launch_bounds__(128) void k_messages(
-    const float* hidden, const int* edges, const int* alist,
-    const float* preW, const float* preb,
-    float* s1, float* s2, unsigned* mxb, unsigned* mnb, const unsigned* ctr){
-  int ne = (int)ctr[1];
-  int tid = threadIdx.x;
-  __shared__ float sd[4][Dd], ss[4][Dd];
-  __shared__ int dsl[4];
-  float pb = preb[tid];
-  for (int j0 = blockIdx.x*4; j0 < ne; j0 += gridDim.x*4){
-    int nv = ne - j0; if (nv > 4) nv = 4;
-    if (tid < 4){
-      int j = j0 + ((tid < nv) ? tid : 0);
-      dsl[tid] = edges[2*j+1];
-    }
-    #pragma unroll
-    for (int e=0;e<4;e++){
-      int j = j0 + ((e < nv) ? e : 0);
-      int s = edges[2*j];
-      int dv = alist[edges[2*j+1]];
-      sd[e][tid] = hidden[(size_t)dv*Dd + tid];
-      ss[e][tid] = hidden[(size_t)s*Dd + tid];
-    }
-    __syncthreads();
-    float a[4] = {pb, pb, pb, pb};
-    #pragma unroll 4
-    for (int k=0;k<Dd;k++){
-      float w0 = preW[k*Dd + tid];
-      float w1 = preW[(Dd+k)*Dd + tid];
-      #pragma unroll
-      for (int e=0;e<4;e++) a[e] += sd[e][k]*w0 + ss[e][k]*w1;
-    }
-    for (int e=0;e<nv;e++){
-      int dslot = dsl[e];
-      atomicAdd(&s1[dslot*Dd + tid], a[e]);
-      atomicAdd(&s2[dslot*Dd + tid], a[e]*a[e]);
-      atomicMax(&mxb[dslot*Dd + tid], encf(a[e]));
-      atomicMin(&mnb[dslot*Dd + tid], encf(a[e]));
-    }
-    __syncthreads();
-  }
-}
-
-__global__ __launch_bounds__(512) void k_post(
-    const unsigned* cnt, const float* s1, const float* s2,
-    const unsigned* mxb, const unsigned* mnb, const float* slot_deg,
-    const float* postW, float* tpart, const unsigned* ctr){
-  int na = (int)ctr[0];
-  int bid = blockIdx.x;
-  int tile = bid & 63, ch = bid >> 6;
-  if (tile*32 >= na) return;
-  float logsum = __uint_as_float(ctr[2]);
-  float avg = (logsum + (float)(BN - na)*LN2F) / (float)BN;
-  __shared__ float lb[32*136];
-  __shared__ float wbuf[3*16*128];
-  __shared__ float sden[32];
-  __shared__ unsigned shas[32];
-  int tid = threadIdx.x;
-  if (tid < 32){
-    unsigned c = cnt[tile*32 + tid];
-    sden[tid] = fmaxf((float)c, 1.0f);
-    shas[tid] = c;
-  }
-  __syncthreads();
-  for (int idx = tid; idx < 32*Dd; idx += 512){
-    int sl = idx >> 7, kk = idx & 127;
-    int gi = (tile*32 + sl)*Dd + kk;
-    float den = sden[sl];
-    float val;
-    if (ch == 0)      val = s1[gi]/den;
-    else if (ch == 1) val = shas[sl] ? decf(mxb[gi]) : 0.f;
-    else if (ch == 2) val = shas[sl] ? decf(mnb[gi]) : 0.f;
-    else {
-      float mv = s1[gi]/den;
-      float var = s2[gi]/den - mv*mv;
-      val = sqrtf(fmaxf(var, 0.f) + EPSV);
-    }
-    lb[sl*136 + kk] = val;
-  }
-  int cg = tid & 31, rg = tid >> 5;
-  int c0 = cg*4;
-  float a0[2][4], a1[2][4], a2[2][4];
-  #pragma unroll
-  for (int i=0;i<2;i++)
-    #pragma unroll
-    for (int j=0;j<4;j++){ a0[i][j]=0.f; a1[i][j]=0.f; a2[i][j]=0.f; }
-  for (int chunk = 0; chunk < 8; ++chunk){
-    #pragma unroll
-    for (int i = 0; i < 3; ++i){
-      int f = tid + i*512;
-      int q = f >> 9, r = f & 511;
-      int kk = r >> 5, c4 = r & 31;
-      int grow = q*512 + ch*128 + chunk*16 + kk;
-      ((float4*)wbuf)[f] = *(const float4*)(postW + (size_t)grow*Dd + c4*4);
-    }
-    __syncthreads();
-    #pragma unroll
-    for (int k4 = 0; k4 < 4; ++k4){
-      float4 av0 = *(const float4*)&lb[(rg*2+0)*136 + chunk*16 + k4*4];
-      float4 av1 = *(const float4*)&lb[(rg*2+1)*136 + chunk*16 + k4*4];
-      #pragma unroll
-      for (int j = 0; j < 4; ++j){
-        int kk = k4*4 + j;
-        float4 w0 = *(const float4*)&wbuf[kk*128 + c0];
-        float4 w1 = *(const float4*)&wbuf[(16+kk)*128 + c0];
-        float4 w2 = *(const float4*)&wbuf[(32+kk)*128 + c0];
-        float av[2] = { (&av0.x)[j], (&av1.x)[j] };
-        #pragma unroll
-        for (int i=0;i<2;i++){
-          float a = av[i];
-          a0[i][0] += a*w0.x; a0[i][1] += a*w0.y; a0[i][2] += a*w0.z; a0[i][3] += a*w0.w;
-          a1[i][0] += a*w1.x; a1[i][1] += a*w1.y; a1[i][2] += a*w1.z; a1[i][3] += a*w1.w;
-          a2[i][0] += a*w2.x; a2[i][1] += a*w2.y; a2[i][2] += a*w2.z; a2[i][3] += a*w2.w;
-        }
-      }
-    }
-    __syncthreads();
-  }
-  #pragma unroll
-  for (int i=0;i<2;i++){
-    int slot = tile*32 + rg*2 + i;
-    if (slot < na){
-      float dg = slot_deg[slot];
-      float logd = logf(dg + 1.f);
-      float al = logd/avg, be = avg/logd;
-      float4 r;
-      r.x = a0[i][0] + al*a1[i][0] + be*a2[i][0];
-      r.y = a0[i][1] + al*a1[i][1] + be*a2[i][1];
-      r.z = a0[i][2] + al*a1[i][2] + be*a2[i][2];
-      r.w = a0[i][3] + al*a1[i][3] + be*a2[i][3];
-      *(float4*)(tpart + (size_t)ch*MAXACT*Dd + (size_t)slot*Dd + c0) = r;
-    }
-  }
-}
-
-__global__ __launch_bounds__(256) void k_out_resid(
-    const float* tpart, const int* alist, const float* outW, const float* outb,
-    const float* postb, float* hidden, const unsigned* ctr){
-  int na = (int)ctr[0];
-  int tile = blockIdx.x;
-  if (tile*32 >= na) return;
-  __shared__ float tr[32*136];
-  __shared__ float wbuf[16*128];
-  int tid = threadIdx.x;
-  for (int idx = tid; idx < 32*Dd; idx += 256){
-    int sl = idx >> 7, kk = idx & 127;
-    size_t o = (size_t)(tile*32 + sl)*Dd + kk;
-    tr[sl*136 + kk] = tpart[o] + tpart[(size_t)MAXACT*Dd + o]
-                    + tpart[(size_t)2*MAXACT*Dd + o] + tpart[(size_t)3*MAXACT*Dd + o]
-                    + postb[kk];
-  }
-  int cg = tid & 31, rg = tid >> 5;
-  int c0 = cg*4;
-  float4 ob = *(const float4*)(outb + c0);
-  float acc[4][4];
-  #pragma unroll
-  for (int r=0;r<4;r++){ acc[r][0]=ob.x; acc[r][1]=ob.y; acc[r][2]=ob.z; acc[r][3]=ob.w; }
-  for (int chunk = 0; chunk < 8; ++chunk){
-    #pragma unroll
-    for (int i = 0; i < 2; ++i){
-      int f = tid + i*256;
-      int kk = f >> 5, c4 = f & 31;
-      ((float4*)wbuf)[f] = *(const float4*)(outW + (size_t)(chunk*16 + kk)*Dd + c4*4);
-    }
-    __syncthreads();
-    #pragma unroll
-    for (int k4 = 0; k4 < 4; ++k4){
-      float4 av[4];
-      #pragma unroll
-      for (int r=0;r<4;r++)
-        av[r] = *(const float4*)&tr[(rg*4+r)*136 + chunk*16 + k4*4];
-      #pragma unroll
-      for (int j = 0; j < 4; ++j){
-        float4 w = *(const float4*)&wbuf[(k4*4+j)*128 + c0];
-        #pragma unroll
-        for (int r=0;r<4;r++){
-          float a = (&av[r].x)[j];
-          acc[r][0] += a*w.x; acc[r][1] += a*w.y; acc[r][2] += a*w.z; acc[r][3] += a*w.w;
-        }
-      }
-    }
-    __syncthreads();
-  }
-  #pragma unroll
-  for (int r=0;r<4;r++){
-    int slot = tile*32 + rg*4 + r;
-    if (slot < na){
-      int v = alist[slot];
-      float* hp = hidden + (size_t)v*Dd + c0;
-      float4 h4 = *(float4*)hp;
-      h4.x += acc[r][0]; h4.y += acc[r][1]; h4.z += acc[r][2]; h4.w += acc[r][3];
-      *(float4*)hp = h4;
-    }
-  }
-}
-
-__global__ __launch_bounds__(256) void k_score(
-    const float* hidden, const float* cvec, const float* linW,
-    const float* m1W, const float* m1b, const float* m2W, const float* m2b,
-    const int* tlist, const unsigned* ctr, float* score,
-    const int* ovr, int ovr_n){
-  int nt = (ovr_n > 0) ? ovr_n : (int)ctr[3];
-  const int* list = (ovr_n > 0) ? ovr : tlist;
-  int nb = blockIdx.x * 32;
-  if (nb >= nt) return;
-  __shared__ float sh[32*Dd];
-  __shared__ float sx[32*Dd];
-  __shared__ float sc[2*Dd];
-  __shared__ int   sv[32];
-  __shared__ float red[32*33];
-  int tid = threadIdx.x;
-  if (tid < 32){
-    int idx = nb + tid;
-    sv[tid] = (idx < nt) ? list[idx] : list[nb];
-  }
-  sc[tid] = cvec[tid];
-  __syncthreads();
-  for (int q = tid; q < 32*32; q += 256){
-    int row = q >> 5, f4 = q & 31;
-    ((float4*)sh)[row*32 + f4] = ((const float4*)(hidden + (size_t)sv[row]*Dd))[f4];
-  }
-  __syncthreads();
-  int cg = tid & 31, rg = tid >> 5;
-  int c0 = cg*4;
-  float acc[4][4];
-  #pragma unroll
-  for (int i=0;i<4;i++){ acc[i][0]=0.f; acc[i][1]=0.f; acc[i][2]=0.f; acc[i][3]=0.f; }
-  for (int k4=0;k4<32;k4++){
-    float4 av[4];
-    #pragma unroll
-    for (int i=0;i<4;i++) av[i] = ((float4*)sh)[(rg*4+i)*32 + k4];
-    #pragma unroll
-    for (int j=0;j<4;j++){
-      float4 w = *(const float4*)(linW + (size_t)(k4*4+j)*Dd + c0);
-      #pragma unroll
-      for (int i=0;i<4;i++){
-        float a = (&av[i].x)[j];
-        acc[i][0] += a*w.x; acc[i][1] += a*w.y; acc[i][2] += a*w.z; acc[i][3] += a*w.w;
-      }
-    }
-  }
-  #pragma unroll
-  for (int i=0;i<4;i++){
-    int row = rg*4 + i;
-    int bb = (sv[row] >= Nn) ? 1 : 0;
-    float4 cv = *(float4*)&sc[bb*Dd + c0];
-    float4 hv = ((float4*)sh)[row*32 + cg];
-    float4 x;
-    x.x = (acc[i][0] + cv.x)*hv.x;
-    x.y = (acc[i][1] + cv.y)*hv.y;
-    x.z = (acc[i][2] + cv.z)*hv.z;
-    x.w = (acc[i][3] + cv.w)*hv.w;
-    ((float4*)sx)[row*32 + cg] = x;
-  }
-  __syncthreads();
-  #pragma unroll
-  for (int i=0;i<4;i++){ acc[i][0]=0.f; acc[i][1]=0.f; acc[i][2]=0.f; acc[i][3]=0.f; }
-  for (int k4=0;k4<32;k4++){
-    float4 av[4];
-    #pragma unroll
-    for (int i=0;i<4;i++) av[i] = ((float4*)sx)[(rg*4+i)*32 + k4];
-    #pragma unroll
-    for (int j=0;j<4;j++){
-      float4 w = *(const float4*)(m1W + (size_t)(k4*4+j)*Dd + c0);
-      #pragma unroll
-      for (int i=0;i<4;i++){
-        float a = (&av[i].x)[j];
-        acc[i][0] += a*w.x; acc[i][1] += a*w.y; acc[i][2] += a*w.z; acc[i][3] += a*w.w;
-      }
-    }
-  }
-  float4 mb = *(const float4*)(m1b + c0);
-  float4 mw = *(const float4*)(m2W + c0);
-  #pragma unroll
-  for (int i=0;i<4;i++){
-    float p0 = fmaxf(acc[i][0]+mb.x, 0.f)*mw.x;
-    float p1 = fmaxf(acc[i][1]+mb.y, 0.f)*mw.y;
-    float p2 = fmaxf(acc[i][2]+mb.z, 0.f)*mw.z;
-    float p3 = fmaxf(acc[i][3]+mb.w, 0.f)*mw.w;
-    red[(rg*4+i)*33 + cg] = p0+p1+p2+p3;
-  }
-  __syncthreads();
-  if (tid < 32){
-    float s = m2b[0];
-    for (int g=0; g<32; g++) s += red[tid*33 + g];
-    if (nb + tid < nt) score[sv[tid]] = s;
-  }
-}
-
-__global__ void k_gather(const float* score, const int* hdr, float* out){
-  int i = threadIdx.x;
-  if (i < Bq*NEG) out[i] = score[hdr[4+i]];
+
+  if (bid == 0 && tid < Bq*NEG) out[tid] = score[hdr[4 + tid]];
 }
 
 extern "C" void kernel_launch(void* const* d_in, const int* in_sizes, int n_in,
@@ -584,61 +635,24 @@
   const float* post_b = (const float*)d_in[15];
   const float* out_W  = (const float*)d_in[16];
   const float* out_b  = (const float*)d_in[17];
-
   char* ws = (char*)d_ws;
-  float*    hidden   = (float*)(ws + HID_OFF);
-  float*    score    = (float*)(ws + SCORE_OFF);
-  float*    cvec     = (float*)(ws + CVEC_OFF);
-  int*      hdr      = (int*)(ws + HDR_OFF);
-  unsigned long long* thr = (unsigned long long*)(ws + THR_OFF);
-  unsigned* sel      = (unsigned*)(ws + SEL_OFF);
-  unsigned* out_deg  = (unsigned*)(ws + DEG_OFF);
-  int*      node_slot= (int*)(ws + SLOT_OFF);
-  unsigned* cnt      = (unsigned*)(ws + CNT_OFF);
-  float*    slot_deg = (float*)(ws + SDEG_OFF);
-  float*    s1       = (float*)(ws + S1_OFF);
-  float*    s2       = (float*)(ws + S2_OFF);
-  unsigned* mxb      = (unsigned*)(ws + MXB_OFF);
-  unsigned* mnb      = (unsigned*)(ws + MNB_OFF);
-  float*    tpart    = (float*)(ws + TPART_OFF);
-  int*      alist    = (int*)(ws + ALIST_OFF);
-  unsigned* flag     = (unsigned*)(ws + FLAG_OFF);
-  int*      tlist    = (int*)(ws + TLIST_OFF);
-  int*      edges    = (int*)(ws + EDGE_OFF);
-  unsigned* ctr      = (unsigned*)(ws + CTR_OFF);
-
-  k_zero<<<(BN*Dd/4 + 255)/256, 256, 0, stream>>>(hidden, flag);
-  k_prep<<<1, 256, 0, stream>>>(h_index, r_index, t_index, hidden_states, rel_embedding,
-                                lin_W, lin_b, m1_W, m1_b, m2_W, m2_b,
-                                hdr, cvec, hidden, score, flag, tlist, ctr);
-  for (int l = 0; l < Ll; ++l){
-    const float* preWl  = pre_W  + (size_t)l*2*Dd*Dd;
-    const float* prebl  = pre_b  + (size_t)l*Dd;
-    const float* postWl = post_W + (size_t)l*12*Dd*Dd;
-    const float* postbl = post_b + (size_t)l*Dd;
-    const float* outWl  = out_W  + (size_t)l*Dd*Dd;
-    const float* outbl  = out_b  + (size_t)l*Dd;
-
-    k_select<<<Bq, 256, 0, stream>>>(score, tlist, ctr, thr);
-    k_mask<<<(MAXACT*Dd + 255)/256, 256, 0, stream>>>(score, thr, sel, out_deg,
-                                                      s1, s2, mxb, mnb, cnt, ctr);
-    k_degree<<<(Ee + 255)/256, 256, 0, stream>>>(edge_index, sel, out_deg);
-    k_active<<<(BN + 255)/256, 256, 0, stream>>>(out_deg, node_slot, alist, slot_deg,
-                                                 ctr, flag, tlist);
-    k_edges<<<(Ee + 255)/256, 256, 0, stream>>>(edge_index, sel, out_deg, node_slot,
-                                                edges, cnt, ctr);
-    k_messages<<<512, 128, 0, stream>>>(hidden, edges, alist, preWl, prebl,
-                                        s1, s2, mxb, mnb, ctr);
-    k_post<<<256, 512, 0, stream>>>(cnt, s1, s2, mxb, mnb, slot_deg, postWl, tpart, ctr);
-    k_out_resid<<<MAXACT/32, 256, 0, stream>>>(tpart, alist, outWl, outbl, postbl,
-                                               hidden, ctr);
-    if (l < Ll-1){
-      k_score<<<MAXTOUCH/32, 256, 0, stream>>>(hidden, cvec, lin_W, m1_W, m1_b, m2_W, m2_b,
-                                               tlist, ctr, score, tlist, 0);
-    } else {
-      k_score<<<1, 256, 0, stream>>>(hidden, cvec, lin_W, m1_W, m1_b, m2_W, m2_b,
-                                     tlist, ctr, score, hdr + 4, Bq*NEG);
-    }
+  float* outp = (float*)d_out;
+
+  static int grid_blocks = 0;
+  if (grid_blocks == 0){
+    int nb = 0;
+    if (hipOccupancyMaxActiveBlocksPerMultiprocessor(&nb, k_main, 256, 0) != hipSuccess || nb < 1)
+      nb = 1;
+    grid_blocks = (nb >= 2) ? 512 : 256;
   }
-  k_gather<<<1, 64, 0, stream>>>(score, hdr, (float*)d_out);
+
+  void* args[] = {
+    (void*)&h_index, (void*)&r_index, (void*)&t_index,
+    (void*)&hidden_states, (void*)&edge_index, (void*)&rel_embedding,
+    (void*)&lin_W, (void*)&lin_b, (void*)&m1_W, (void*)&m1_b,
+    (void*)&m2_W, (void*)&m2_b, (void*)&pre_W, (void*)&pre_b,
+    (void*)&post_W, (void*)&post_b, (void*)&out_W, (void*)&out_b,
+    (void*)&ws, (void*)&outp
+  };
+  hipLaunchCooperativeKernel((void*)k_main, dim3(grid_blocks), dim3(256), args, 0, stream);
 }
```
